# Kernel optimization log

Hardware: AMD Instinct MI355X
Metric: run time of the kernel (lower is better)

## Reference

```python
import jax, jax.numpy as jnp
import numpy as np

B, N, C, NH = 4, 2304, 256, 8
HD = C // NH            # head dim = 32
HS = WS = 48            # H = W = sqrt(N)
RADIUS = 3.0
MLP_HID = 4 * C
SCALE = HD ** (-0.5)
NEG = -1e9              # stands in for -inf (identical softmax up to fp eps)
EPS = 1e-6


def spatial_mask():
    # get_spatial_mask: cdist of (y, x) grid coords, -inf where dist > radius
    yy, xx = jnp.meshgrid(jnp.arange(HS), jnp.arange(WS), indexing='ij')
    coords = jnp.stack([yy, xx], -1).reshape(-1, 2).astype(jnp.float32)  # [N, 2]
    d2 = jnp.sum((coords[:, None, :] - coords[None, :, :]) ** 2, -1)     # [N, N]
    return jnp.where(d2 > RADIUS * RADIUS, NEG, 0.0)


def layernorm(x, g, b):
    mu = jnp.mean(x, -1, keepdims=True)
    var = jnp.mean((x - mu) ** 2, -1, keepdims=True)
    return (x - mu) * jax.lax.rsqrt(var + EPS) * g + b


def setup_inputs() -> dict:
    key = jax.random.key(0)
    ks = jax.random.split(key, 16)
    s = 0.02
    return {
        'x':    jax.random.normal(ks[0], (B, N, C), jnp.float32),
        'x_kv': jax.random.normal(ks[1], (B, N, C), jnp.float32),
        'Wq': jax.random.normal(ks[2], (C, C), jnp.float32) * s,
        'bq': jnp.zeros((C,), jnp.float32),
        'Wk': jax.random.normal(ks[3], (C, C), jnp.float32) * s,
        'bk': jnp.zeros((C,), jnp.float32),
        'Wv': jax.random.normal(ks[4], (C, C), jnp.float32) * s,
        'bv': jnp.zeros((C,), jnp.float32),
        'Wp': jax.random.normal(ks[5], (C, C), jnp.float32) * s,
        'bp': jnp.zeros((C,), jnp.float32),
        'g1': jnp.ones((C,), jnp.float32),
        'b1': jnp.zeros((C,), jnp.float32),
        'g2': jnp.ones((C,), jnp.float32),
        'b2': jnp.zeros((C,), jnp.float32),
        'W1': jax.random.normal(ks[6], (C, MLP_HID), jnp.float32) * s,
        'bm1': jnp.zeros((MLP_HID,), jnp.float32),
        'W2': jax.random.normal(ks[7], (MLP_HID, C), jnp.float32) * s,
        'bm2': jnp.zeros((C,), jnp.float32),
    }


def reference(x, x_kv, Wq, bq, Wk, bk, Wv, bv, Wp, bp,
              g1, b1, g2, b2, W1, bm1, W2, bm2):
    mask = spatial_mask()                                  # [N, N]
    h = layernorm(x, g1, b1)
    hkv = layernorm(x_kv, g1, b1)
    q = (h @ Wq + bq).reshape(B, N, NH, HD)
    k = (hkv @ Wk + bk).reshape(B, N, NH, HD)
    v = (hkv @ Wv + bv).reshape(B, N, NH, HD)
    scores = jnp.einsum('bqhd,bkhd->bhqk', q, k) * SCALE + mask
    attn = jax.nn.softmax(scores, axis=-1)
    out = jnp.einsum('bhqk,bkhd->bqhd', attn, v).reshape(B, N, C)
    x = x + out @ Wp + bp
    m = layernorm(x, g2, b2)
    x = x + jax.nn.gelu(m @ W1 + bm1, approximate=False) @ W2 + bm2
    return x
```

## Files before the change

kernel.cpp:

```cpp
#include <hip/hip_runtime.h>
#include <hip/hip_fp16.h>
#include <math.h>

#define BB 4
#define NN 2304
#define CC 256
#define HS 48
#define HID 1024
#define BNROWS (BB * NN)
#define ATTN_SCALE 0.17677669529663687f

typedef _Float16 f16;
typedef __attribute__((ext_vector_type(2))) _Float16 h2;
typedef __attribute__((ext_vector_type(8))) _Float16 h8;
typedef __attribute__((ext_vector_type(4))) float f4;

#define GLLS16(g, l)                                                        \
    __builtin_amdgcn_global_load_lds(                                       \
        (const __attribute__((address_space(1))) unsigned int*)(g),         \
        (__attribute__((address_space(3))) unsigned int*)(l), 16, 0, 0)
#define WAIT_VM0()   asm volatile("s_waitcnt vmcnt(0)" ::: "memory")
#define WAIT_VM4()   asm volatile("s_waitcnt vmcnt(4)" ::: "memory")
#define WAIT_VM5()   asm volatile("s_waitcnt vmcnt(5)" ::: "memory")
#define WAIT_VM6()   asm volatile("s_waitcnt vmcnt(6)" ::: "memory")
#define WAIT_LGKM0() asm volatile("s_waitcnt lgkmcnt(0)" ::: "memory")

static __device__ __forceinline__ float wave_sum64(float v) {
    v += __shfl_xor(v, 32, 64);
    v += __shfl_xor(v, 16, 64);
    v += __shfl_xor(v, 8, 64);
    v += __shfl_xor(v, 4, 64);
    v += __shfl_xor(v, 2, 64);
    v += __shfl_xor(v, 1, 64);
    return v;
}

static __device__ __forceinline__ int xcd_swizzle_lin() {
    const int gx = (int)gridDim.x;
    const int lin = (int)blockIdx.y * gx + (int)blockIdx.x;
    const int nwg = gx * (int)gridDim.y;
    return (nwg & 7) ? lin : ((lin & 7) * (nwg >> 3) + (lin >> 3));
}

__global__ __launch_bounds__(256) void prep_ln1_kernel(
    const float* __restrict__ x, const float* __restrict__ xkv,
    const float* __restrict__ Wq, const float* __restrict__ Wk,
    const float* __restrict__ Wv, const float* __restrict__ Wp,
    const float* __restrict__ W1, const float* __restrict__ W2,
    const float* __restrict__ bq, const float* __restrict__ bk,
    const float* __restrict__ bv,
    const float* __restrict__ g, const float* __restrict__ be,
    f16* __restrict__ WqkvT, f16* __restrict__ WpT,
    f16* __restrict__ W1T, f16* __restrict__ W2T, float* __restrict__ bqkv,
    f16* __restrict__ hq, f16* __restrict__ hkv)
{
    __shared__ float tt[32][33];
    int bx = blockIdx.x;
    const int tid = threadIdx.x;
    if (bx < 768) {
        const float* src; f16* dst; int K, N;
        if (bx < 64)        { src = Wq; dst = WqkvT;           K = 256;  N = 256; }
        else if (bx < 128)  { src = Wk; dst = WqkvT + 65536;   K = 256;  N = 256;  bx -= 64; }
        else if (bx < 192)  { src = Wv; dst = WqkvT + 131072;  K = 256;  N = 256;  bx -= 128; }
        else if (bx < 256)  { src = Wp; dst = WpT;             K = 256;  N = 256;  bx -= 192; }
        else if (bx < 512)  { src = W1; dst = W1T;             K = 256;  N = 1024; bx -= 256; }
        else                { src = W2; dst = W2T;             K = 1024; N = 256;  bx -= 512; }
        const int tN = N >> 5;
        const int kt = bx / tN, nt = bx - kt * tN;
        const int rr = tid >> 5, cc = tid & 31;
#pragma unroll
        for (int j = 0; j < 4; ++j)
            tt[rr + 8 * j][cc] = src[(size_t)(kt * 32 + rr + 8 * j) * N + nt * 32 + cc];
        __syncthreads();
#pragma unroll
        for (int j = 0; j < 4; ++j)
            dst[(size_t)(nt * 32 + rr + 8 * j) * K + kt * 32 + cc] = (f16)tt[cc][rr + 8 * j];
        return;
    }
    if (bx == 768) {
        if (tid < 256) {
            bqkv[tid]       = bq[tid];
            bqkv[tid + 256] = bk[tid];
            bqkv[tid + 512] = bv[tid];
        }
        return;
    }
    const int r = (bx - 769) * 4 + (tid >> 6);
    const int lane = tid & 63;
    const float* src; f16* dst;
    if (r < BNROWS) { src = x + (size_t)r * CC;              dst = hq + (size_t)r * CC; }
    else { src = xkv + (size_t)(r - BNROWS) * CC; dst = hkv + (size_t)(r - BNROWS) * CC; }
    const float4 v = ((const float4*)src)[lane];
    const float mu = wave_sum64(v.x + v.y + v.z + v.w) * (1.0f / CC);
    const float d0 = v.x - mu, d1 = v.y - mu, d2 = v.z - mu, d3 = v.w - mu;
    const float var = wave_sum64(d0 * d0 + d1 * d1 + d2 * d2 + d3 * d3) * (1.0f / CC);
    const float rs = rsqrtf(var + 1e-6f);
    const float4 g4 = ((const float4*)g)[lane];
    const float4 b4 = ((const float4*)be)[lane];
    h2 o01 = (h2){(f16)(d0 * rs * g4.x + b4.x), (f16)(d1 * rs * g4.y + b4.y)};
    h2 o23 = (h2){(f16)(d2 * rs * g4.z + b4.z), (f16)(d3 * rs * g4.w + b4.w)};
    ((h2*)dst)[lane * 2] = o01;
    ((h2*)dst)[lane * 2 + 1] = o23;
}

template <bool GELU, int RESID, bool OUTF32, bool QKV>
__global__ __launch_bounds__(256, 4) void gemm_wave(
    const f16* __restrict__ Aq, const f16* __restrict__ Akv,
    const f16* __restrict__ Bt, const float* __restrict__ bias,
    const void* __restrict__ resid, void* __restrict__ out1,
    void* __restrict__ outkv, int N, int K)
{
    __shared__ f16 lds[4 * 6144];
    const int tid = threadIdx.x;
    const int wid = tid >> 6, lane = tid & 63;
    const int ln15 = lane & 15, quad = lane >> 4;
    const int jr = lane >> 2, js = lane & 3;
    f16* slot = lds + wid * 6144;
    const int sl = xcd_swizzle_lin();
    const int gx = (int)gridDim.x;
    const int bx = sl % gx, by = sl / gx;
    const int n0 = bx * 64;
    const int m0 = (by * 4 + wid) * 32;
    const f16* Ap = QKV ? (n0 < 256 ? Aq : Akv) : Aq;

    size_t ga[2], gb[4];
#pragma unroll
    for (int i = 0; i < 2; ++i) {
        const int r = i * 16 + jr;
        const int q = (js - (r >> 1)) & 3;
        ga[i] = (size_t)(m0 + r) * K + q * 8;
    }
#pragma unroll
    for (int i = 0; i < 4; ++i) {
        const int r = i * 16 + jr;
        const int q = (js - (r >> 1)) & 3;
        gb[i] = (size_t)(n0 + r) * K + q * 8;
    }
    int aoff[2], boff[4];
#pragma unroll
    for (int mt = 0; mt < 2; ++mt) {
        const int r = mt * 16 + ln15;
        aoff[mt] = (r * 4 + ((quad + (r >> 1)) & 3)) * 16;
    }
#pragma unroll
    for (int nt = 0; nt < 4; ++nt) {
        const int r = nt * 16 + ln15;
        boff[nt] = (r * 4 + ((quad + (r >> 1)) & 3)) * 16;
    }

    f4 acc[2][4];
#pragma unroll
    for (int i = 0; i < 2; ++i)
#pragma unroll
        for (int j = 0; j < 4; ++j) acc[i][j] = (f4){0.f, 0.f, 0.f, 0.f};

    {
        f16* Al = slot;
        f16* Bl = slot + 1024;
#pragma unroll
        for (int i = 0; i < 2; ++i) GLLS16(Ap + ga[i], Al + i * 512);
#pragma unroll
        for (int i = 0; i < 4; ++i) GLLS16(Bt + gb[i], Bl + i * 512);
    }

    int cur = 0;
    for (int k0 = 0; k0 < K; k0 += 32) {
        const bool more = (k0 + 32 < K);
        f16* Ac = slot + cur * 3072;
        f16* Bc = Ac + 1024;
        if (more) {
            f16* An = slot + (cur ^ 1) * 3072;
            f16* Bn = An + 1024;
            WAIT_LGKM0();
#pragma unroll
            for (int i = 0; i < 2; ++i) GLLS16(Ap + ga[i] + k0 + 32, An + i * 512);
#pragma unroll
            for (int i = 0; i < 4; ++i) GLLS16(Bt + gb[i] + k0 + 32, Bn + i * 512);
            WAIT_VM6();
        } else {
            WAIT_VM0();
        }
        h8 aF[2], bF[4];
#pragma unroll
        for (int nt = 0; nt < 4; ++nt)
            bF[nt] = *(const h8*)((const char*)Bc + boff[nt]);
#pragma unroll
        for (int mt = 0; mt < 2; ++mt)
            aF[mt] = *(const h8*)((const char*)Ac + aoff[mt]);
#pragma unroll
        for (int mt = 0; mt < 2; ++mt)
#pragma unroll
            for (int nt = 0; nt < 4; ++nt)
                acc[mt][nt] = __builtin_amdgcn_mfma_f32_16x16x32_f16(
                    aF[mt], bF[nt], acc[mt][nt], 0, 0, 0);
        cur ^= 1;
    }

    f16* qdst = nullptr; int qstr = 0, qn0 = 0;
    if (QKV) {
        if (n0 < 256) { qdst = (f16*)out1;  qstr = 256; qn0 = n0; }
        else          { qdst = (f16*)outkv; qstr = 512; qn0 = n0 - 256; }
    }
#pragma unroll
    for (int nt = 0; nt < 4; ++nt) {
        const int gn = n0 + nt * 16 + ln15;
        const float bs = bias[gn];
#pragma unroll
        for (int mt = 0; mt < 2; ++mt) {
#pragma unroll
            for (int r = 0; r < 4; ++r) {
                const int gm = m0 + mt * 16 + quad * 4 + r;
                float v = acc[mt][nt][r] + bs;
                if (GELU) v = 0.5f * v * (1.0f + erff(v * 0.70710678118654752f));
                if (RESID == 1) v += ((const float*)resid)[(size_t)gm * N + gn];
                if (RESID == 2) v += (float)((const f16*)resid)[(size_t)gm * N + gn];
                if (QKV) {
                    qdst[(size_t)gm * qstr + qn0 + nt * 16 + ln15] = (f16)v;
                } else if (OUTF32) {
                    ((float*)out1)[(size_t)gm * N + gn] = v;
                } else {
                    ((f16*)out1)[(size_t)gm * N + gn] = (f16)v;
                }
            }
        }
    }
}

__global__ __launch_bounds__(256, 4) void gemm_op_ln2(
    const f16* __restrict__ Aa, const f16* __restrict__ Bt,
    const float* __restrict__ bias, const float* __restrict__ xres,
    const float* __restrict__ g, const float* __restrict__ be,
    f16* __restrict__ x1, f16* __restrict__ m2)
{
    __shared__ f16 lds[4 * 5120];
    __shared__ float sred[16][4][2];
    const int tid = threadIdx.x;
    const int wid = tid >> 6, lane = tid & 63;
    const int ln15 = lane & 15, quad = lane >> 4;
    const int jr = lane >> 2, js = lane & 3;
    f16* slot = lds + wid * 5120;
    const int m0 = blockIdx.x * 16;
    const int n0 = wid * 64;
    const int K = 256;

    size_t ga, gb[4];
    {
        const int q = (js - (jr >> 1)) & 3;
        ga = (size_t)(m0 + jr) * K + q * 8;
    }
#pragma unroll
    for (int i = 0; i < 4; ++i) {
        const int r = i * 16 + jr;
        const int q = (js - (r >> 1)) & 3;
        gb[i] = (size_t)(n0 + r) * K + q * 8;
    }
    const int aoff = (ln15 * 4 + ((quad + (ln15 >> 1)) & 3)) * 16;
    int boff[4];
#pragma unroll
    for (int nt = 0; nt < 4; ++nt) {
        const int r = nt * 16 + ln15;
        boff[nt] = (r * 4 + ((quad + (r >> 1)) & 3)) * 16;
    }

    f4 acc[4];
#pragma unroll
    for (int j = 0; j < 4; ++j) acc[j] = (f4){0.f, 0.f, 0.f, 0.f};

    {
        f16* Al = slot;
        f16* Bl = slot + 512;
        GLLS16(Aa + ga, Al);
#pragma unroll
        for (int i = 0; i < 4; ++i) GLLS16(Bt + gb[i], Bl + i * 512);
    }
    int cur = 0;
    for (int k0 = 0; k0 < K; k0 += 32) {
        const bool more = (k0 + 32 < K);
        f16* Ac = slot + cur * 2560;
        f16* Bc = Ac + 512;
        if (more) {
            f16* An = slot + (cur ^ 1) * 2560;
            f16* Bn = An + 512;
            WAIT_LGKM0();
            GLLS16(Aa + ga + k0 + 32, An);
#pragma unroll
            for (int i = 0; i < 4; ++i) GLLS16(Bt + gb[i] + k0 + 32, Bn + i * 512);
            WAIT_VM5();
        } else {
            WAIT_VM0();
        }
        h8 aF, bF[4];
#pragma unroll
        for (int nt = 0; nt < 4; ++nt)
            bF[nt] = *(const h8*)((const char*)Bc + boff[nt]);
        aF = *(const h8*)((const char*)Ac + aoff);
#pragma unroll
        for (int nt = 0; nt < 4; ++nt)
            acc[nt] = __builtin_amdgcn_mfma_f32_16x16x32_f16(
                aF, bF[nt], acc[nt], 0, 0, 0);
        cur ^= 1;
    }

    float bsv[4], g2v[4], b2v[4];
#pragma unroll
    for (int nt = 0; nt < 4; ++nt) {
        const int gn = n0 + nt * 16 + ln15;
        bsv[nt] = bias[gn];
        g2v[nt] = g[gn];
        b2v[nt] = be[gn];
    }
    float s1[4], s2[4];
#pragma unroll
    for (int r = 0; r < 4; ++r) { s1[r] = 0.f; s2[r] = 0.f; }
#pragma unroll
    for (int r = 0; r < 4; ++r) {
        const int gm = m0 + quad * 4 + r;
#pragma unroll
        for (int nt = 0; nt < 4; ++nt) {
            const int gn = n0 + nt * 16 + ln15;
            float v = acc[nt][r] + bsv[nt] + xres[(size_t)gm * CC + gn];
            acc[nt][r] = v;
            x1[(size_t)gm * CC + gn] = (f16)v;
            s1[r] += v;
            s2[r] += v * v;
        }
    }
#pragma unroll
    for (int off = 1; off < 16; off <<= 1) {
#pragma unroll
        for (int r = 0; r < 4; ++r) {
            s1[r] += __shfl_xor(s1[r], off, 64);
            s2[r] += __shfl_xor(s2[r], off, 64);
        }
    }
    if (ln15 == 0) {
#pragma unroll
        for (int r = 0; r < 4; ++r) {
            const int rr = quad * 4 + r;
            sred[rr][wid][0] = s1[r];
            sred[rr][wid][1] = s2[r];
        }
    }
    __syncthreads();
#pragma unroll
    for (int r = 0; r < 4; ++r) {
        const int rr = quad * 4 + r;
        const int gm = m0 + rr;
        float a = 0.f, b = 0.f;
#pragma unroll
        for (int w = 0; w < 4; ++w) {
            a += sred[rr][w][0];
            b += sred[rr][w][1];
        }
        const float mu = a * (1.0f / CC);
        const float var = fmaxf(b * (1.0f / CC) - mu * mu, 0.0f);
        const float rs = rsqrtf(var + 1e-6f);
#pragma unroll
        for (int nt = 0; nt < 4; ++nt) {
            const int gn = n0 + nt * 16 + ln15;
            const float v = acc[nt][r];
            m2[(size_t)gm * CC + gn] = (f16)((v - mu) * rs * g2v[nt] + b2v[nt]);
        }
    }
}

__global__ __launch_bounds__(256, 3) void mlp_fused(
    const f16* __restrict__ m2g, const f16* __restrict__ W1T,
    const f16* __restrict__ W2T, const float* __restrict__ bm1,
    const float* __restrict__ bm2, const f16* __restrict__ x1,
    float* __restrict__ outp)
{
    __shared__ f16 lds[4 * 5120];
    __shared__ f16 hbuf[16 * 256];
    const int tid = threadIdx.x;
    const int wid = tid >> 6, lane = tid & 63;
    const int ln15 = lane & 15, quad = lane >> 4;
    const int jr = lane >> 2, js = lane & 3;
    f16* slot = lds + wid * 5120;
    const int m0 = blockIdx.x * 16;

    size_t ga;
    {
        const int q = (js - (jr >> 1)) & 3;
        ga = (size_t)(m0 + jr) * 256 + q * 8;
    }
    size_t gb1[4];
#pragma unroll
    for (int i = 0; i < 4; ++i) {
        const int r = i * 16 + jr;
        const int q = (js - (r >> 1)) & 3;
        gb1[i] = (size_t)(wid * 64 + r) * 256 + q * 8;
    }
    size_t gb2[4];
#pragma unroll
    for (int i = 0; i < 4; ++i) {
        const int r = i * 16 + jr;
        const int q = (js - (r >> 1)) & 3;
        gb2[i] = (size_t)(wid * 64 + r) * 1024 + q * 8;
    }
    const int aoff = (ln15 * 4 + ((quad + (ln15 >> 1)) & 3)) * 16;
    int boff[4];
#pragma unroll
    for (int nt = 0; nt < 4; ++nt) {
        const int r = nt * 16 + ln15;
        boff[nt] = (r * 4 + ((quad + (r >> 1)) & 3)) * 16;
    }

    f4 acc2[4];
#pragma unroll
    for (int j = 0; j < 4; ++j) acc2[j] = (f4){0.f, 0.f, 0.f, 0.f};

#pragma unroll 1
    for (int qt = 0; qt < 4; ++qt) {
        const size_t w1ofs = (size_t)qt * 65536;
        {
            f16* Al = slot;
            f16* Bl = slot + 512;
            GLLS16(m2g + ga, Al);
#pragma unroll
            for (int i = 0; i < 4; ++i)
                GLLS16(W1T + gb1[i] + w1ofs, Bl + i * 512);
        }
        int cur = 0;
        f4 accp[4];
#pragma unroll
        for (int j = 0; j < 4; ++j) accp[j] = (f4){0.f, 0.f, 0.f, 0.f};
#pragma unroll 1
        for (int it = 0; it < 8; ++it) {
            f16* Ac = slot + cur * 2560;
            f16* Bc = Ac + 512;
            if (it < 7) {
                f16* An = slot + (cur ^ 1) * 2560;
                f16* Bn = An + 512;
                WAIT_LGKM0();
                GLLS16(m2g + ga + (it + 1) * 32, An);
#pragma unroll
                for (int i = 0; i < 4; ++i)
                    GLLS16(W1T + gb1[i] + w1ofs + (it + 1) * 32, Bn + i * 512);
                WAIT_VM5();
            } else {
                WAIT_VM0();
            }
            h8 aF, bF[4];
#pragma unroll
            for (int nt = 0; nt < 4; ++nt)
                bF[nt] = *(const h8*)((const char*)Bc + boff[nt]);
            aF = *(const h8*)((const char*)Ac + aoff);
#pragma unroll
            for (int nt = 0; nt < 4; ++nt)
                accp[nt] = __builtin_amdgcn_mfma_f32_16x16x32_f16(
                    aF, bF[nt], accp[nt], 0, 0, 0);
            cur ^= 1;
        }
#pragma unroll
        for (int nt = 0; nt < 4; ++nt)
#pragma unroll
            for (int r = 0; r < 4; ++r) {
                const int row = quad * 4 + r;
                const int col = wid * 64 + nt * 16 + ln15;
                float v = accp[nt][r] + bm1[qt * 256 + col];
                v = 0.5f * v * (1.0f + erff(v * 0.70710678118654752f));
                const int sw = (col >> 3) ^ (row & 7);
                hbuf[row * 256 + sw * 8 + (col & 7)] = (f16)v;
            }
        __syncthreads();
        {
            f16* Bl = slot;
#pragma unroll
            for (int i = 0; i < 4; ++i)
                GLLS16(W2T + gb2[i] + qt * 256, Bl + i * 512);
        }
        cur = 0;
#pragma unroll 1
        for (int it = 0; it < 8; ++it) {
            f16* Bc = slot + cur * 2048;
            if (it < 7) {
                f16* Bn = slot + (cur ^ 1) * 2048;
                WAIT_LGKM0();
#pragma unroll
                for (int i = 0; i < 4; ++i)
                    GLLS16(W2T + gb2[i] + qt * 256 + (it + 1) * 32, Bn + i * 512);
                WAIT_VM4();
            } else {
                WAIT_VM0();
            }
            h8 bF[4];
#pragma unroll
            for (int nt = 0; nt < 4; ++nt)
                bF[nt] = *(const h8*)((const char*)Bc + boff[nt]);
            h8 aF;
            {
                const int g = (it * 4 + quad) ^ (ln15 & 7);
                aF = *(const h8*)&hbuf[ln15 * 256 + g * 8];
            }
#pragma unroll
            for (int nt = 0; nt < 4; ++nt)
                acc2[nt] = __builtin_amdgcn_mfma_f32_16x16x32_f16(
                    aF, bF[nt], acc2[nt], 0, 0, 0);
            cur ^= 1;
        }
        if (qt < 3) __syncthreads();
    }
#pragma unroll
    for (int nt = 0; nt < 4; ++nt) {
        const int gn = wid * 64 + nt * 16 + ln15;
        const float bs = bm2[gn];
#pragma unroll
        for (int r = 0; r < 4; ++r) {
            const int gm = m0 + quad * 4 + r;
            const float v = acc2[nt][r] + bs + (float)x1[(size_t)gm * CC + gn];
            outp[(size_t)gm * CC + gn] = v;
        }
    }
}

__device__ __constant__ int ATT_DY[29] = {
    -3, -2, -2, -2, -2, -2, -1, -1, -1, -1, -1, 0, 0, 0, 0,
    0, 0, 0, 1, 1, 1, 1, 1, 2, 2, 2, 2, 2, 3};
__device__ __constant__ int ATT_DX[29] = {
    0, -2, -1, 0, 1, 2, -2, -1, 0, 1, 2, -3, -2, -1, 0,
    1, 2, 3, -2, -1, 0, 1, 2, -2, -1, 0, 1, 2, 0};

__global__ __launch_bounds__(128) void attn_tile_kernel(
    const f16* __restrict__ qf, const f16* __restrict__ kvf,
    f16* __restrict__ ao)
{
    __shared__ f16 ks[196][66];
    __shared__ f16 vs[196][66];
    const int tile = blockIdx.x, hp = blockIdx.y, b = blockIdx.z;
    const int ty0 = (tile / 6) * 8, tx0 = (tile - (tile / 6) * 6) * 8;
    const int tid = threadIdx.x;

    const int q = tid & 63, hh = tid >> 6;
    const int qy = q >> 3, qx = q & 7;
    const size_t qrow = (size_t)b * NN + (ty0 + qy) * HS + tx0 + qx;
    const f16* qp = qf + qrow * CC + hp * 64 + hh * 32;
    uint4 qa[4];
#pragma unroll
    for (int i = 0; i < 4; ++i) qa[i] = ((const uint4*)qp)[i];

#pragma unroll
    for (int bt = 0; bt < 5; ++bt) {
        uint4 v[5];
        int rr[5], sg[5];
#pragma unroll
        for (int j = 0; j < 5; ++j) {
            const int it = bt * 5 + j;
            const int idx = tid + it * 128;
            const int r = idx >> 4, seg = idx & 15;
            rr[j] = r; sg[j] = seg;
            const int ry = r / 14;
            const int gy = ty0 - 3 + ry, gx = tx0 - 3 + (r - ry * 14);
            uint4 val = {0u, 0u, 0u, 0u};
            const bool act = (it < 24) || (tid < 64);
            if (act && (unsigned)gy < HS && (unsigned)gx < HS) {
                const size_t rowb = ((size_t)b * NN + gy * HS + gx) * 512;
                const int ch = (seg < 8) ? (hp * 64 + seg * 8)
                                         : (256 + hp * 64 + (seg - 8) * 8);
                val = *(const uint4*)&kvf[rowb + ch];
            }
            v[j] = val;
        }
#pragma unroll
        for (int j = 0; j < 5; ++j) {
            const int it = bt * 5 + j;
            if (it == 24 && tid >= 64) continue;
            f16* dstp = (sg[j] < 8) ? &ks[rr[j]][(sg[j] & 7) * 8]
                                    : &vs[rr[j]][(sg[j] & 7) * 8];
            ((unsigned int*)dstp)[0] = v[j].x;
            ((unsigned int*)dstp)[1] = v[j].y;
            ((unsigned int*)dstp)[2] = v[j].z;
            ((unsigned int*)dstp)[3] = v[j].w;
        }
    }
    __syncthreads();

    const h2* q2 = (const h2*)qa;

    float s[29];
#pragma unroll
    for (int n = 0; n < 29; ++n) {
        const int dy = ATT_DY[n], dx = ATT_DX[n];
        const int r = (qy + 3 + dy) * 14 + qx + 3 + dx;
        const bool valid = (unsigned)(ty0 + qy + dy) < HS &&
                           (unsigned)(tx0 + qx + dx) < HS;
        float a = 0.0f;
        const h2* kp = (const h2*)&ks[r][hh * 32];
#pragma unroll
        for (int i = 0; i < 16; ++i)
            a = __builtin_amdgcn_fdot2(q2[i], kp[i], a, false);
        s[n] = valid ? a * ATTN_SCALE : -1e30f;
    }
    float m = s[0];
#pragma unroll
    for (int n = 1; n < 29; ++n) m = fmaxf(m, s[n]);
    float l = 0.0f;
#pragma unroll
    for (int n = 0; n < 29; ++n) { s[n] = __expf(s[n] - m); l += s[n]; }
    h2 a2[16];
#pragma unroll
    for (int i = 0; i < 16; ++i) a2[i] = (h2){(f16)0.f, (f16)0.f};
#pragma unroll
    for (int n = 0; n < 29; ++n) {
        const int dy = ATT_DY[n], dx = ATT_DX[n];
        const int r = (qy + 3 + dy) * 14 + qx + 3 + dx;
        const f16 pn = (f16)s[n];
        const h2 ph = (h2){pn, pn};
        const h2* vp = (const h2*)&vs[r][hh * 32];
#pragma unroll
        for (int i = 0; i < 16; ++i) a2[i] += ph * vp[i];
    }
    const float inv = 1.0f / l;
    uint4 ov[4];
    f16* oh = (f16*)ov;
#pragma unroll
    for (int i = 0; i < 16; ++i) {
        oh[2 * i]     = (f16)((float)a2[i][0] * inv);
        oh[2 * i + 1] = (f16)((float)a2[i][1] * inv);
    }
    uint4* dst = (uint4*)(ao + qrow * CC + hp * 64 + hh * 32);
#pragma unroll
    for (int i = 0; i < 4; ++i) dst[i] = ov[i];
}

extern "C" void kernel_launch(void* const* d_in, const int* in_sizes, int n_in,
                              void* d_out, int out_size, void* d_ws, size_t ws_size,
                              hipStream_t stream) {
    const float* x    = (const float*)d_in[0];
    const float* x_kv = (const float*)d_in[1];
    const float* Wq   = (const float*)d_in[2];
    const float* bq   = (const float*)d_in[3];
    const float* Wk   = (const float*)d_in[4];
    const float* bk   = (const float*)d_in[5];
    const float* Wv   = (const float*)d_in[6];
    const float* bv   = (const float*)d_in[7];
    const float* Wp   = (const float*)d_in[8];
    const float* bp   = (const float*)d_in[9];
    const float* g1   = (const float*)d_in[10];
    const float* b1   = (const float*)d_in[11];
    const float* g2   = (const float*)d_in[12];
    const float* b2   = (const float*)d_in[13];
    const float* W1   = (const float*)d_in[14];
    const float* bm1  = (const float*)d_in[15];
    const float* W2   = (const float*)d_in[16];
    const float* bm2  = (const float*)d_in[17];
    float* outp = (float*)d_out;

    f16* wsh = (f16*)d_ws;
    f16* WqkvT = wsh;
    f16* WpT   = wsh + 196608;
    f16* W1T   = wsh + 262144;
    f16* W2T   = wsh + 524288;
    float* bqkv = (float*)(wsh + 786432);
    f16* hq    = wsh + 787968;
    f16* hkv   = wsh + 3147264;
    f16* qf    = wsh + 5506560;
    f16* kvf   = wsh + 7865856;
    f16* ao    = hq;
    f16* x1    = hkv;
    f16* m2    = qf;

    prep_ln1_kernel<<<5377, 256, 0, stream>>>(
        x, x_kv, Wq, Wk, Wv, Wp, W1, W2, bq, bk, bv, g1, b1,
        WqkvT, WpT, W1T, W2T, bqkv, hq, hkv);
    gemm_wave<false, 0, false, true><<<dim3(12, 72), 256, 0, stream>>>(
        hq, hkv, WqkvT, bqkv, nullptr, qf, kvf, 768, 256);
    attn_tile_kernel<<<dim3(36, 4, BB), 128, 0, stream>>>(qf, kvf, ao);
    gemm_op_ln2<<<576, 256, 0, stream>>>(ao, WpT, bp, x, g2, b2, x1, m2);
    mlp_fused<<<576, 256, 0, stream>>>(m2, W1T, W2T, bm1, bm2, x1, outp);
    (void)in_sizes; (void)n_in; (void)out_size; (void)ws_size;
}
```

Baseline: 184.9 us.

## Split fused MLP into two tiled 128-row block GEMMs with materialized hidden

Replaces the fused per-16-row MLP kernel, where each block streamed all of W1 and W2 for only 16 rows, with two separate block-tiled GEMM launches (128-row tiles). The first computes GELU(m2·W1+b) into a fp16 hidden buffer and the second adds W2 plus bias and residual. The goal is much higher weight reuse per block and better MFMA utilization, at the cost of writing and reading an 8x1024 hidden activation through global memory. When the workspace is too small it falls back to per-batch launches.

```diff
diff --git a/kernel.cpp b/kernel.cpp
--- a/kernel.cpp
+++ b/kernel.cpp
@@ -20,7 +20,6 @@
         (const __attribute__((address_space(1))) unsigned int*)(g),         \
         (__attribute__((address_space(3))) unsigned int*)(l), 16, 0, 0)
 #define WAIT_VM0()   asm volatile("s_waitcnt vmcnt(0)" ::: "memory")
-#define WAIT_VM4()   asm volatile("s_waitcnt vmcnt(4)" ::: "memory")
 #define WAIT_VM5()   asm volatile("s_waitcnt vmcnt(5)" ::: "memory")
 #define WAIT_VM6()   asm volatile("s_waitcnt vmcnt(6)" ::: "memory")
 #define WAIT_LGKM0() asm volatile("s_waitcnt lgkmcnt(0)" ::: "memory")
@@ -364,152 +363,101 @@
     }
 }
 
-__global__ __launch_bounds__(256, 3) void mlp_fused(
-    const f16* __restrict__ m2g, const f16* __restrict__ W1T,
-    const f16* __restrict__ W2T, const float* __restrict__ bm1,
-    const float* __restrict__ bm2, const f16* __restrict__ x1,
-    float* __restrict__ outp)
+template <int BN, int WGM, int WGN, bool GELU, bool FINAL>
+__global__ __launch_bounds__(256, 2) void gemm_block(
+    const f16* __restrict__ A, const f16* __restrict__ Bt,
+    const float* __restrict__ bias, const f16* __restrict__ resid16,
+    void* __restrict__ outv, int N, int K)
 {
-    __shared__ f16 lds[4 * 5120];
-    __shared__ f16 hbuf[16 * 256];
+    constexpr int T = 8 + BN / 16;
+    constexpr int BUFE = 128 * 32 + BN * 32;
+    constexpr int MT = 128 / WGM / 16;
+    constexpr int WM = 128 / WGM, WN = BN / WGN;
+    __shared__ f16 lds[2 * BUFE];
     const int tid = threadIdx.x;
     const int wid = tid >> 6, lane = tid & 63;
     const int ln15 = lane & 15, quad = lane >> 4;
     const int jr = lane >> 2, js = lane & 3;
-    f16* slot = lds + wid * 5120;
-    const int m0 = blockIdx.x * 16;
-
-    size_t ga;
-    {
-        const int q = (js - (jr >> 1)) & 3;
-        ga = (size_t)(m0 + jr) * 256 + q * 8;
-    }
-    size_t gb1[4];
-#pragma unroll
-    for (int i = 0; i < 4; ++i) {
-        const int r = i * 16 + jr;
-        const int q = (js - (r >> 1)) & 3;
-        gb1[i] = (size_t)(wid * 64 + r) * 256 + q * 8;
-    }
-    size_t gb2[4];
-#pragma unroll
-    for (int i = 0; i < 4; ++i) {
-        const int r = i * 16 + jr;
-        const int q = (js - (r >> 1)) & 3;
-        gb2[i] = (size_t)(wid * 64 + r) * 1024 + q * 8;
-    }
-    const int aoff = (ln15 * 4 + ((quad + (ln15 >> 1)) & 3)) * 16;
-    int boff[4];
+    const int wr = (WGN == 1) ? wid : (wid >> 1);
+    const int wc = (WGN == 1) ? 0 : (wid & 1);
+
+    const int sl = xcd_swizzle_lin();
+    const int gx = (int)gridDim.x;
+    const int m0 = (sl % gx) * 128;
+    const int n0 = (sl / gx) * BN;
+
+    const size_t gabase = (size_t)jr * K + (size_t)(((js - (jr >> 1)) & 3) * 8);
+
+    int aoff[MT], boff[4];
+#pragma unroll
+    for (int mt = 0; mt < MT; ++mt) {
+        const int rr = wr * WM + mt * 16 + ln15;
+        aoff[mt] = (rr * 4 + ((quad + (rr >> 1)) & 3)) * 16;
+    }
 #pragma unroll
     for (int nt = 0; nt < 4; ++nt) {
-        const int r = nt * 16 + ln15;
-        boff[nt] = (r * 4 + ((quad + (r >> 1)) & 3)) * 16;
-    }
-
-    f4 acc2[4];
-#pragma unroll
-    for (int j = 0; j < 4; ++j) acc2[j] = (f4){0.f, 0.f, 0.f, 0.f};
-
-#pragma unroll 1
-    for (int qt = 0; qt < 4; ++qt) {
-        const size_t w1ofs = (size_t)qt * 65536;
-        {
-            f16* Al = slot;
-            f16* Bl = slot + 512;
-            GLLS16(m2g + ga, Al);
-#pragma unroll
-            for (int i = 0; i < 4; ++i)
-                GLLS16(W1T + gb1[i] + w1ofs, Bl + i * 512);
-        }
-        int cur = 0;
-        f4 accp[4];
-#pragma unroll
-        for (int j = 0; j < 4; ++j) accp[j] = (f4){0.f, 0.f, 0.f, 0.f};
-#pragma unroll 1
-        for (int it = 0; it < 8; ++it) {
-            f16* Ac = slot + cur * 2560;
-            f16* Bc = Ac + 512;
-            if (it < 7) {
-                f16* An = slot + (cur ^ 1) * 2560;
-                f16* Bn = An + 512;
-                WAIT_LGKM0();
-                GLLS16(m2g + ga + (it + 1) * 32, An);
-#pragma unroll
-                for (int i = 0; i < 4; ++i)
-                    GLLS16(W1T + gb1[i] + w1ofs + (it + 1) * 32, Bn + i * 512);
-                WAIT_VM5();
-            } else {
-                WAIT_VM0();
+        const int rr = wc * WN + nt * 16 + ln15;
+        boff[nt] = 8192 + (rr * 4 + ((quad + (rr >> 1)) & 3)) * 16;
+    }
+
+    f4 acc[MT][4];
+#pragma unroll
+    for (int i = 0; i < MT; ++i)
+#pragma unroll
+        for (int j = 0; j < 4; ++j) acc[i][j] = (f4){0.f, 0.f, 0.f, 0.f};
+
+#define GB_STAGE(dst, kk)                                                     \
+    _Pragma("unroll")                                                         \
+    for (int i = 0; i < T / 4; ++i) {                                         \
+        const int g = wid + i * 4;                                            \
+        const size_t rowoff =                                                 \
+            (size_t)((g & 8) ? (n0 + (g & 7) * 16) : (m0 + g * 16)) * K;      \
+        const f16* sp = ((g & 8) ? Bt : A) + rowoff + gabase + (kk);          \
+        GLLS16(sp, (dst) + g * 512);                                          \
+    }
+
+    GB_STAGE(lds, 0);
+    __syncthreads();
+    int cur = 0;
+    for (int k0 = 0; k0 < K; k0 += 32) {
+        f16* bufc = lds + cur * BUFE;
+        if (k0 + 32 < K) { GB_STAGE(lds + (cur ^ 1) * BUFE, k0 + 32); }
+        h8 aF[MT], bF[4];
+#pragma unroll
+        for (int nt = 0; nt < 4; ++nt)
+            bF[nt] = *(const h8*)((const char*)bufc + boff[nt]);
+#pragma unroll
+        for (int mt = 0; mt < MT; ++mt)
+            aF[mt] = *(const h8*)((const char*)bufc + aoff[mt]);
+#pragma unroll
+        for (int mt = 0; mt < MT; ++mt)
+#pragma unroll
+            for (int nt = 0; nt < 4; ++nt)
+                acc[mt][nt] = __builtin_amdgcn_mfma_f32_16x16x32_f16(
+                    aF[mt], bF[nt], acc[mt][nt], 0, 0, 0);
+        __syncthreads();
+        cur ^= 1;
+    }
+#undef GB_STAGE
+
+#pragma unroll
+    for (int nt = 0; nt < 4; ++nt) {
+        const int gn = n0 + wc * WN + nt * 16 + ln15;
+        const float bs = bias[gn];
+#pragma unroll
+        for (int mt = 0; mt < MT; ++mt) {
+#pragma unroll
+            for (int r = 0; r < 4; ++r) {
+                const int gm = m0 + wr * WM + mt * 16 + quad * 4 + r;
+                float v = acc[mt][nt][r] + bs;
+                if (GELU) v = 0.5f * v * (1.0f + erff(v * 0.70710678118654752f));
+                if (FINAL) {
+                    v += (float)resid16[(size_t)gm * N + gn];
+                    ((float*)outv)[(size_t)gm * N + gn] = v;
+                } else {
+                    ((f16*)outv)[(size_t)gm * N + gn] = (f16)v;
+                }
             }
-            h8 aF, bF[4];
-#pragma unroll
-            for (int nt = 0; nt < 4; ++nt)
-                bF[nt] = *(const h8*)((const char*)Bc + boff[nt]);
-            aF = *(const h8*)((const char*)Ac + aoff);
-#pragma unroll
-            for (int nt = 0; nt < 4; ++nt)
-                accp[nt] = __builtin_amdgcn_mfma_f32_16x16x32_f16(
-                    aF, bF[nt], accp[nt], 0, 0, 0);
-            cur ^= 1;
-        }
-#pragma unroll
-        for (int nt = 0; nt < 4; ++nt)
-#pragma unroll
-            for (int r = 0; r < 4; ++r) {
-                const int row = quad * 4 + r;
-                const int col = wid * 64 + nt * 16 + ln15;
-                float v = accp[nt][r] + bm1[qt * 256 + col];
-                v = 0.5f * v * (1.0f + erff(v * 0.70710678118654752f));
-                const int sw = (col >> 3) ^ (row & 7);
-                hbuf[row * 256 + sw * 8 + (col & 7)] = (f16)v;
-            }
-        __syncthreads();
-        {
-            f16* Bl = slot;
-#pragma unroll
-            for (int i = 0; i < 4; ++i)
-                GLLS16(W2T + gb2[i] + qt * 256, Bl + i * 512);
-        }
-        cur = 0;
-#pragma unroll 1
-        for (int it = 0; it < 8; ++it) {
-            f16* Bc = slot + cur * 2048;
-            if (it < 7) {
-                f16* Bn = slot + (cur ^ 1) * 2048;
-                WAIT_LGKM0();
-#pragma unroll
-                for (int i = 0; i < 4; ++i)
-                    GLLS16(W2T + gb2[i] + qt * 256 + (it + 1) * 32, Bn + i * 512);
-                WAIT_VM4();
-            } else {
-                WAIT_VM0();
-            }
-            h8 bF[4];
-#pragma unroll
-            for (int nt = 0; nt < 4; ++nt)
-                bF[nt] = *(const h8*)((const char*)Bc + boff[nt]);
-            h8 aF;
-            {
-                const int g = (it * 4 + quad) ^ (ln15 & 7);
-                aF = *(const h8*)&hbuf[ln15 * 256 + g * 8];
-            }
-#pragma unroll
-            for (int nt = 0; nt < 4; ++nt)
-                acc2[nt] = __builtin_amdgcn_mfma_f32_16x16x32_f16(
-                    aF, bF[nt], acc2[nt], 0, 0, 0);
-            cur ^= 1;
-        }
-        if (qt < 3) __syncthreads();
-    }
-#pragma unroll
-    for (int nt = 0; nt < 4; ++nt) {
-        const int gn = wid * 64 + nt * 16 + ln15;
-        const float bs = bm2[gn];
-#pragma unroll
-        for (int r = 0; r < 4; ++r) {
-            const int gm = m0 + quad * 4 + r;
-            const float v = acc2[nt][r] + bs + (float)x1[(size_t)gm * CC + gn];
-            outp[(size_t)gm * CC + gn] = v;
         }
     }
 }
@@ -659,6 +607,8 @@
     f16* ao    = hq;
     f16* x1    = hkv;
     f16* m2    = qf;
+    f16* hidF  = kvf;
+    const bool fused = ws_size >= (size_t)17303040 * sizeof(f16);
 
     prep_ln1_kernel<<<5377, 256, 0, stream>>>(
         x, x_kv, Wq, Wk, Wv, Wp, W1, W2, bq, bk, bv, g1, b1,
@@ -667,6 +617,19 @@
         hq, hkv, WqkvT, bqkv, nullptr, qf, kvf, 768, 256);
     attn_tile_kernel<<<dim3(36, 4, BB), 128, 0, stream>>>(qf, kvf, ao);
     gemm_op_ln2<<<576, 256, 0, stream>>>(ao, WpT, bp, x, g2, b2, x1, m2);
-    mlp_fused<<<576, 256, 0, stream>>>(m2, W1T, W2T, bm1, bm2, x1, outp);
-    (void)in_sizes; (void)n_in; (void)out_size; (void)ws_size;
-}
+    if (fused) {
+        gemm_block<128, 2, 2, true, false><<<dim3(72, 8), 256, 0, stream>>>(
+            m2, W1T, bm1, nullptr, hidF, HID, 256);
+        gemm_block<64, 4, 1, false, true><<<dim3(72, 4), 256, 0, stream>>>(
+            hidF, W2T, bm2, x1, outp, CC, 1024);
+    } else {
+        for (int b = 0; b < BB; ++b) {
+            const size_t off = (size_t)b * NN * CC;
+            gemm_block<128, 2, 2, true, false><<<dim3(18, 8), 256, 0, stream>>>(
+                m2 + off, W1T, bm1, nullptr, hidF, HID, 256);
+            gemm_block<64, 4, 1, false, true><<<dim3(18, 4), 256, 0, stream>>>(
+                hidF, W2T, bm2, x1 + off, outp + off, CC, 1024);
+        }
+    }
+    (void)in_sizes; (void)n_in; (void)out_size;
+}
```

Result: faster. 179.4 us (-2.9%).
